# Optimization experiments

Hardware: AMD Instinct MI355X
Metric: run time of the kernel (lower is better)

Reference implementation:

```python
import jax, jax.numpy as jnp
import numpy as np

D_MODEL = 512
OUT = 512
D_STATE = 16
D_CONV = 4
EXPAND = 2
N_LAYERS = 2
D_INNER = EXPAND * D_MODEL
DT_RANK = -(-D_MODEL // 16)  # ceil(d_model/16) = 32
B = 2
L = 2048


def setup_inputs() -> dict:
    key = jax.random.key(0)
    ks = jax.random.split(key, 16)
    def w(k, shape, scale):
        return jax.random.normal(k, shape, dtype=jnp.float32) * scale
    s_d = 1.0 / np.sqrt(D_MODEL)
    s_e = 1.0 / np.sqrt(D_INNER)
    s_r = 1.0 / np.sqrt(DT_RANK)
    s_f = 1.0 / np.sqrt(2 * D_MODEL)
    return {
        "x": jax.random.normal(ks[0], (B, L, D_MODEL), dtype=jnp.float32),
        "in_proj_w": w(ks[1], (N_LAYERS, 2 * D_INNER, D_MODEL), s_d),
        "conv_w": w(ks[2], (N_LAYERS, D_INNER, D_CONV), 0.5),
        "conv_b": jnp.zeros((N_LAYERS, D_INNER), jnp.float32),
        "x_proj_w": w(ks[3], (N_LAYERS, DT_RANK + 2 * D_STATE, D_INNER), s_e),
        "dt_w": w(ks[4], (N_LAYERS, D_INNER, DT_RANK), s_r),
        "dt_b": w(ks[5], (N_LAYERS, D_INNER), 0.1),
        "A_log": jnp.tile(jnp.log(jnp.arange(1, D_STATE + 1, dtype=jnp.float32))[None, None, :], (N_LAYERS, D_INNER, 1)),
        "Dp": jnp.ones((N_LAYERS, D_INNER), jnp.float32),
        "out_proj_w": w(ks[6], (N_LAYERS, D_MODEL, D_INNER), s_e),
        "rms_w": jnp.ones((N_LAYERS, D_MODEL), jnp.float32),
        "ln1_w": jnp.ones((D_MODEL,), jnp.float32),
        "ln1_b": jnp.zeros((D_MODEL,), jnp.float32),
        "ln2_w": jnp.ones((D_MODEL,), jnp.float32),
        "ln2_b": jnp.zeros((D_MODEL,), jnp.float32),
        "ffn_w1": w(ks[7], (2 * D_MODEL, D_MODEL), s_d),
        "ffn_b1": jnp.zeros((2 * D_MODEL,), jnp.float32),
        "ffn_w2": w(ks[8], (D_MODEL, 2 * D_MODEL), s_f),
        "ffn_b2": jnp.zeros((D_MODEL,), jnp.float32),
        "final_w": w(ks[9], (OUT, D_MODEL), s_d),
        "final_b": jnp.zeros((OUT,), jnp.float32),
    }


def _ln(x, w, b, eps=1e-5):
    mu = x.mean(-1, keepdims=True)
    v = ((x - mu) ** 2).mean(-1, keepdims=True)
    return (x - mu) * jax.lax.rsqrt(v + eps) * w + b


def _rms(x, w, eps=1e-5):
    return x * jax.lax.rsqrt(jnp.mean(x * x, -1, keepdims=True) + eps) * w


def _mixer(x, ipw, cw, cb, xpw, dtw, dtb, alog, dpar, opw):
    # x: [B, L, D]; single Mamba mixer (in_proj -> causal depthwise conv -> SSM -> gate -> out_proj)
    Lx = x.shape[1]
    xz = x @ ipw.T                              # [B, L, 2*ED]
    xc, z = jnp.split(xz, 2, axis=-1)
    xp = jnp.pad(xc, ((0, 0), (D_CONV - 1, 0), (0, 0)))  # causal left-pad
    xc = cb + sum(cw[:, k] * xp[:, k:k + Lx, :] for k in range(D_CONV))
    xc = jax.nn.silu(xc)
    dbc = xc @ xpw.T                            # [B, L, dt_rank + 2*N]
    delta = jax.nn.softplus(dbc[..., :DT_RANK] @ dtw.T + dtb)   # [B, L, ED]
    Bm = dbc[..., DT_RANK:DT_RANK + D_STATE]    # [B, L, N]
    Cm = dbc[..., DT_RANK + D_STATE:]           # [B, L, N]
    A = -jnp.exp(alog)                          # [ED, N]
    dA = jnp.exp(delta[..., None] * A)          # [B, L, ED, N]
    dBx = (delta * xc)[..., None] * Bm[:, :, None, :]  # [B, L, ED, N]
    def step(h, inp):
        a, bx = inp
        h = a * h + bx
        return h, h
    _, hs = jax.lax.scan(step, jnp.zeros_like(dA[:, 0]), (jnp.moveaxis(dA, 1, 0), jnp.moveaxis(dBx, 1, 0)))
    hs = jnp.moveaxis(hs, 0, 1)                 # [B, L, ED, N]
    y = jnp.einsum('blen,bln->ble', hs, Cm) + dpar * xc
    return (y * jax.nn.silu(z)) @ opw.T


def _forward(x, in_proj_w, conv_w, conv_b, x_proj_w, dt_w, dt_b, A_log, Dp, out_proj_w, rms_w,
             ln1_w, ln1_b, ln2_w, ln2_b, ffn_w1, ffn_b1, ffn_w2, ffn_b2, final_w, final_b):
    h = _ln(x, ln1_w, ln1_b)
    for i in range(N_LAYERS):  # Mamba = stack of residual RMSNorm+mixer blocks
        h = h + _mixer(_rms(h, rms_w[i]), in_proj_w[i], conv_w[i], conv_b[i], x_proj_w[i],
                       dt_w[i], dt_b[i], A_log[i], Dp[i], out_proj_w[i])
    x = x + h
    f = jax.nn.relu(_ln(x, ln2_w, ln2_b) @ ffn_w1.T + ffn_b1) @ ffn_w2.T + ffn_b2
    x = x + f
    return x @ final_w.T + final_b


def reference(x, in_proj_w, conv_w, conv_b, x_proj_w, dt_w, dt_b, A_log, Dp, out_proj_w, rms_w,
              ln1_w, ln1_b, ln2_w, ln2_b, ffn_w1, ffn_b1, ffn_w2, ffn_b2, final_w, final_b):
    return _forward(x, in_proj_w, conv_w, conv_b, x_proj_w, dt_w, dt_b, A_log, Dp, out_proj_w, rms_w,
                    ln1_w, ln1_b, ln2_w, ln2_b, ffn_w1, ffn_b1, ffn_w2, ffn_b2, final_w, final_b)
```

## Files before the change

### kernel.cpp

```cpp
#include <hip/hip_runtime.h>
#include <math.h>

#define ROWS 4096
#define LSEQ 2048
#define DM   512
#define DI   1024
#define NCH  64
#define CHT  (LSEQ / NCH)
#define NCOMB 1152

typedef __bf16 bf16_t;
typedef bf16_t bf16x8 __attribute__((ext_vector_type(8)));
typedef float f32x4 __attribute__((ext_vector_type(4)));
typedef unsigned int u32;
typedef const __attribute__((address_space(1))) u32* gp32;
typedef __attribute__((address_space(3))) u32* lp32;

__device__ __forceinline__ float siluf(float v) { return v / (1.f + expf(-v)); }
__device__ __forceinline__ float softplusf(float v) {
    return fmaxf(v, 0.f) + log1pf(expf(-fabsf(v)));
}

template <bool OUTBF>
__global__ __launch_bounds__(256) void ln_kernel(const float* __restrict__ x,
                                                 const float* __restrict__ w,
                                                 const float* __restrict__ b,
                                                 void* __restrict__ outv) {
    int row = blockIdx.x;
    int tid = threadIdx.x;
    const float* xr = x + (size_t)row * DM;
    float v0 = xr[tid], v1 = xr[tid + 256];
    float sum = v0 + v1, sq = v0 * v0 + v1 * v1;
    for (int o = 32; o > 0; o >>= 1) {
        sum += __shfl_down(sum, o);
        sq  += __shfl_down(sq, o);
    }
    __shared__ float s1[4], s2[4];
    int wid = tid >> 6, lane = tid & 63;
    if (lane == 0) { s1[wid] = sum; s2[wid] = sq; }
    __syncthreads();
    sum = s1[0] + s1[1] + s1[2] + s1[3];
    sq  = s2[0] + s2[1] + s2[2] + s2[3];
    float mu  = sum * (1.f / DM);
    float var = sq * (1.f / DM) - mu * mu;
    float r   = rsqrtf(var + 1e-5f);
    float o0 = (v0 - mu) * r * w[tid] + b[tid];
    float o1 = (v1 - mu) * r * w[tid + 256] + b[tid + 256];
    if (OUTBF) {
        bf16_t* out = (bf16_t*)outv;
        out[(size_t)row * DM + tid]       = (bf16_t)o0;
        out[(size_t)row * DM + tid + 256] = (bf16_t)o1;
    } else {
        float* out = (float*)outv;
        out[(size_t)row * DM + tid]       = o0;
        out[(size_t)row * DM + tid + 256] = o1;
    }
}

__global__ __launch_bounds__(256) void rms_kernel(const float* __restrict__ x,
                                                  const float* __restrict__ w,
                                                  bf16_t* __restrict__ out) {
    int row = blockIdx.x;
    int tid = threadIdx.x;
    const float* xr = x + (size_t)row * DM;
    float v0 = xr[tid], v1 = xr[tid + 256];
    float sq = v0 * v0 + v1 * v1;
    for (int o = 32; o > 0; o >>= 1) sq += __shfl_down(sq, o);
    __shared__ float s2[4];
    int wid = tid >> 6, lane = tid & 63;
    if (lane == 0) s2[wid] = sq;
    __syncthreads();
    sq = s2[0] + s2[1] + s2[2] + s2[3];
    float r = rsqrtf(sq * (1.f / DM) + 1e-5f);
    out[(size_t)row * DM + tid]       = (bf16_t)(v0 * r * w[tid]);
    out[(size_t)row * DM + tid + 256] = (bf16_t)(v1 * r * w[tid + 256]);
}

__global__ __launch_bounds__(256) void cvt_kernel(
    const float* __restrict__ ipw, const float* __restrict__ opw,
    const float* __restrict__ fw1, const float* __restrict__ fw2,
    const float* __restrict__ finw, bf16_t* __restrict__ arena) {
    int idx = blockIdx.x * 256 + threadIdx.x;
    float v;
    if (idx < 2097152)      v = ipw[idx];
    else if (idx < 3145728) v = opw[idx - 2097152];
    else if (idx < 3670016) v = fw1[idx - 3145728];
    else if (idx < 4194304) v = fw2[idx - 3670016];
    else                    v = finw[idx - 4194304];
    arena[idx] = (bf16_t)v;
}

__global__ __launch_bounds__(256) void wd_kernel(
    const float* __restrict__ dtw, const float* __restrict__ xpw,
    bf16_t* __restrict__ wcomb) {
    int idx = blockIdx.x * 256 + threadIdx.x;
    int j = idx & 1023;
    int i = idx >> 10;
    float v;
    if (i < 1024) {
        const float* dr = dtw + i * 32;
        v = 0.f;
#pragma unroll
        for (int k = 0; k < 32; ++k) v = fmaf(dr[k], xpw[k * 1024 + j], v);
    } else if (i < 1056) {
        v = xpw[(i - 1024 + 32) * 1024 + j];
    } else {
        v = 0.f;
    }
    wcomb[idx] = (bf16_t)v;
}

template <int ACT, bool BIAS, bool RES, bool OUTBF>
__global__ __launch_bounds__(256) void mgemm_kernel(
    const bf16_t* __restrict__ A, const bf16_t* __restrict__ W,
    const float* __restrict__ bias, const float* __restrict__ res,
    void* __restrict__ Cv, int M, int N, int K, int ldc,
    const bf16_t* __restrict__ xcp, float* __restrict__ dxc,
    float* __restrict__ bcb, void* __restrict__ aux) {
    __shared__ bf16_t As[128 * 64];
    __shared__ bf16_t Bs[128 * 64];
    const int tid  = threadIdx.x;
    const int lane = tid & 63;
    const int wave = tid >> 6;
    const int wr = wave >> 1, wc = wave & 1;
    const int bm = blockIdx.y * 128, bn = blockIdx.x * 128;
    const int l16 = lane & 15, kgrp = lane >> 4;
    const int prow = tid >> 3;
    const int pp   = tid & 7;
    const int wbase = (tid & ~63) * 8;

    f32x4 acc[4][4] = {};

    for (int k0 = 0; k0 < K; k0 += 64) {
        __syncthreads();
#pragma unroll
        for (int it = 0; it < 4; ++it) {
            int r  = it * 32 + prow;
            int gc = k0 + ((pp ^ (r & 7)) << 3);
            const bf16_t* ga = A + (size_t)(bm + r) * K + gc;
            const bf16_t* gb = W + (size_t)(bn + r) * K + gc;
            __builtin_amdgcn_global_load_lds((gp32)(const void*)ga,
                (lp32)(void*)(As + it * 2048 + wbase), 16, 0, 0);
            __builtin_amdgcn_global_load_lds((gp32)(const void*)gb,
                (lp32)(void*)(Bs + it * 2048 + wbase), 16, 0, 0);
        }
        __syncthreads();
#pragma unroll
        for (int ks = 0; ks < 2; ++ks) {
            bf16x8 af[4], bv[4];
#pragma unroll
            for (int i = 0; i < 4; ++i) {
                int ra = wr * 64 + i * 16 + l16;
                int rb = wc * 64 + i * 16 + l16;
                af[i] = *(const bf16x8*)(As + ra * 64 + ((((ks << 2) | kgrp) ^ (ra & 7)) << 3));
                bv[i] = *(const bf16x8*)(Bs + rb * 64 + ((((ks << 2) | kgrp) ^ (rb & 7)) << 3));
            }
#pragma unroll
            for (int i = 0; i < 4; ++i)
#pragma unroll
                for (int j = 0; j < 4; ++j)
                    acc[i][j] = __builtin_amdgcn_mfma_f32_16x16x32_bf16(
                        af[i], bv[j], acc[i][j], 0, 0, 0);
        }
    }
#pragma unroll
    for (int i = 0; i < 4; ++i) {
#pragma unroll
        for (int j = 0; j < 4; ++j) {
            int col = bn + wc * 64 + j * 16 + l16;
            if (ACT == 2) {
                if (col < 1024) {
                    float badd = bias[col];
#pragma unroll
                    for (int q = 0; q < 4; ++q) {
                        int row = bm + wr * 64 + i * 16 + kgrp * 4 + q;
                        float d = softplusf(acc[i][j][q] + badd);
                        ((float*)Cv)[(size_t)row * 1024 + col] = d;
                        dxc[(size_t)row * 1024 + col] =
                            d * (float)xcp[(size_t)row * 1024 + col];
                    }
                } else if (col < 1056) {
#pragma unroll
                    for (int q = 0; q < 4; ++q) {
                        int row = bm + wr * 64 + i * 16 + kgrp * 4 + q;
                        bcb[(size_t)row * 32 + (col - 1024)] = acc[i][j][q];
                    }
                }
            } else if (ACT == 3) {
#pragma unroll
                for (int q = 0; q < 4; ++q) {
                    int row = bm + wr * 64 + i * 16 + kgrp * 4 + q;
                    float v = acc[i][j][q];
                    if (col < 1024)
                        ((float*)Cv)[(size_t)row * 1024 + col] = v;
                    else
                        ((bf16_t*)aux)[(size_t)row * 1024 + (col - 1024)] = (bf16_t)v;
                }
            } else {
                float badd = BIAS ? bias[col] : 0.f;
#pragma unroll
                for (int q = 0; q < 4; ++q) {
                    int row = bm + wr * 64 + i * 16 + kgrp * 4 + q;
                    float v = acc[i][j][q] + badd;
                    if (RES) v += res[(size_t)row * ldc + col];
                    if (ACT == 1) v = fmaxf(v, 0.f);
                    if (OUTBF) ((bf16_t*)Cv)[(size_t)row * ldc + col] = (bf16_t)v;
                    else       ((float*)Cv)[(size_t)row * ldc + col] = v;
                }
            }
        }
    }
}

__global__ __launch_bounds__(256) void conv_silu_kernel(
    const float* __restrict__ xraw, const float* __restrict__ cw,
    const float* __restrict__ cb, bf16_t* __restrict__ out) {
    int idx = blockIdx.x * blockDim.x + threadIdx.x;
    int c = idx & (DI - 1);
    int row = idx >> 10;
    int t = row & (LSEQ - 1);
    float acc = cb[c];
#pragma unroll
    for (int k = 0; k < 4; ++k) {
        int st = t + k - 3;
        if (st >= 0) acc = fmaf(cw[c * 4 + k], xraw[(size_t)(row + k - 3) * 1024 + c], acc);
    }
    out[idx] = (bf16_t)siluf(acc);
}

__global__ __launch_bounds__(256) void scan1_kernel(
    const float* __restrict__ dbuf, const float* __restrict__ dxcb,
    const float* __restrict__ bc_in, const float* __restrict__ A_log,
    float* __restrict__ aprod, float* __restrict__ bacc) {
    int gid  = blockIdx.x * 256 + threadIdx.x;
    int e    = gid >> 1;
    int half = gid & 1;
    int ch = blockIdx.y;
    int b  = blockIdx.z;
    float cAn[8];
#pragma unroll
    for (int n = 0; n < 8; ++n)
        cAn[n] = -expf(A_log[e * 16 + half * 8 + n]) * 1.4426950408889634f;
    float ap[8], bc[8];
#pragma unroll
    for (int n = 0; n < 8; ++n) { ap[n] = 1.f; bc[n] = 0.f; }
    int row0 = b * LSEQ + ch * CHT;
    float d_c   = dbuf[(size_t)row0 * DI + e];
    float dxc_c = dxcb[(size_t)row0 * 1024 + e];
    for (int t = 0; t < CHT; ++t) {
        int row = row0 + t;
        float d_n = 0.f, dxc_n = 0.f;
        if (t + 1 < CHT) {
            d_n   = dbuf[(size_t)(row + 1) * DI + e];
            dxc_n = dxcb[(size_t)(row + 1) * 1024 + e];
        }
        const float* brow = bc_in + (size_t)row * 32 + half * 8;
        float4 b0 = *(const float4*)brow;
        float4 b1 = *(const float4*)(brow + 4);
        float Bn[8] = {b0.x, b0.y, b0.z, b0.w, b1.x, b1.y, b1.z, b1.w};
#pragma unroll
        for (int n = 0; n < 8; ++n) {
            float dA = exp2f(d_c * cAn[n]);
            ap[n] *= dA;
            bc[n] = fmaf(dA, bc[n], dxc_c * Bn[n]);
        }
        d_c = d_n; dxc_c = dxc_n;
    }
    size_t idx = ((size_t)((b * NCH + ch) * DI + e)) * 16 + half * 8;
    float4* apo = (float4*)(aprod + idx);
    float4* bco = (float4*)(bacc + idx);
#pragma unroll
    for (int q = 0; q < 2; ++q) {
        apo[q] = make_float4(ap[q * 4], ap[q * 4 + 1], ap[q * 4 + 2], ap[q * 4 + 3]);
        bco[q] = make_float4(bc[q * 4], bc[q * 4 + 1], bc[q * 4 + 2], bc[q * 4 + 3]);
    }
}

__global__ __launch_bounds__(256) void scan2_kernel(
    const float* aprod, const float* bacc, float* hinit) {
    int tid = blockIdx.x * 256 + threadIdx.x;
    int n = tid & 15;
    int e = (tid >> 4) & (DI - 1);
    int b = tid >> 14;
    float h = 0.f;
    for (int ch = 0; ch < NCH; ++ch) {
        size_t idx = ((size_t)((b * NCH + ch) * DI + e)) * 16 + n;
        float a  = aprod[idx];
        float bb = bacc[idx];
        hinit[idx] = h;
        h = fmaf(a, h, bb);
    }
}

__global__ __launch_bounds__(256) void scan3_kernel(
    const float* __restrict__ dbuf, const float* __restrict__ dxcb,
    const bf16_t* __restrict__ xcb, const bf16_t* __restrict__ zb,
    const float* __restrict__ bc_in, const float* __restrict__ A_log,
    const float* __restrict__ Dp, const float* __restrict__ hinit,
    bf16_t* __restrict__ yg) {
    int gid  = blockIdx.x * 256 + threadIdx.x;
    int e    = gid >> 1;
    int half = gid & 1;
    int ch = blockIdx.y;
    int b  = blockIdx.z;
    float cAn[8];
#pragma unroll
    for (int n = 0; n < 8; ++n)
        cAn[n] = -expf(A_log[e * 16 + half * 8 + n]) * 1.4426950408889634f;
    float h[8];
    {
        const float4* hp = (const float4*)(hinit +
            ((size_t)((b * NCH + ch) * DI + e)) * 16 + half * 8);
#pragma unroll
        for (int q = 0; q < 2; ++q) {
            float4 v = hp[q];
            h[q * 4] = v.x; h[q * 4 + 1] = v.y; h[q * 4 + 2] = v.z; h[q * 4 + 3] = v.w;
        }
    }
    float Dpe = Dp[e];
    int row0 = b * LSEQ + ch * CHT;
    float d_c   = dbuf[(size_t)row0 * DI + e];
    float dxc_c = dxcb[(size_t)row0 * 1024 + e];
    float xc_c  = (float)xcb[(size_t)row0 * 1024 + e];
    float z_c   = (float)zb[(size_t)row0 * 1024 + e];
    for (int t = 0; t < CHT; ++t) {
        int row = row0 + t;
        float d_n = 0.f, dxc_n = 0.f, xc_n = 0.f, z_n = 0.f;
        if (t + 1 < CHT) {
            d_n   = dbuf[(size_t)(row + 1) * DI + e];
            dxc_n = dxcb[(size_t)(row + 1) * 1024 + e];
            xc_n  = (float)xcb[(size_t)(row + 1) * 1024 + e];
            z_n   = (float)zb[(size_t)(row + 1) * 1024 + e];
        }
        const float* brow = bc_in + (size_t)row * 32;
        float4 b0 = *(const float4*)(brow + half * 8);
        float4 b1 = *(const float4*)(brow + half * 8 + 4);
        float4 c0 = *(const float4*)(brow + 16 + half * 8);
        float4 c1 = *(const float4*)(brow + 16 + half * 8 + 4);
        float Bn[8] = {b0.x, b0.y, b0.z, b0.w, b1.x, b1.y, b1.z, b1.w};
        float Cn[8] = {c0.x, c0.y, c0.z, c0.w, c1.x, c1.y, c1.z, c1.w};
        float y = half ? 0.f : Dpe * xc_c;
#pragma unroll
        for (int n = 0; n < 8; ++n) {
            float dA = exp2f(d_c * cAn[n]);
            h[n] = fmaf(dA, h[n], dxc_c * Bn[n]);
            y = fmaf(h[n], Cn[n], y);
        }
        y += __shfl_xor(y, 1);
        if (half == 0)
            yg[(size_t)row * DI + e] = (bf16_t)(y * siluf(z_c));
        d_c = d_n; dxc_c = dxc_n; xc_c = xc_n; z_c = z_n;
    }
}

__global__ __launch_bounds__(256) void add_kernel(const float* __restrict__ a,
                                                  const float* __restrict__ b,
                                                  float* __restrict__ c, int n) {
    int i = blockIdx.x * blockDim.x + threadIdx.x;
    if (i < n) c[i] = a[i] + b[i];
}

extern "C" void kernel_launch(void* const* d_in, const int* in_sizes, int n_in,
                              void* d_out, int out_size, void* d_ws, size_t ws_size,
                              hipStream_t stream) {
    const float* x    = (const float*)d_in[0];
    const float* ipw  = (const float*)d_in[1];
    const float* cw   = (const float*)d_in[2];
    const float* cb   = (const float*)d_in[3];
    const float* xpw  = (const float*)d_in[4];
    const float* dtw  = (const float*)d_in[5];
    const float* dtb  = (const float*)d_in[6];
    const float* alog = (const float*)d_in[7];
    const float* dpar = (const float*)d_in[8];
    const float* opw  = (const float*)d_in[9];
    const float* rmsw = (const float*)d_in[10];
    const float* ln1w = (const float*)d_in[11];
    const float* ln1b = (const float*)d_in[12];
    const float* ln2w = (const float*)d_in[13];
    const float* ln2b = (const float*)d_in[14];
    const float* fw1  = (const float*)d_in[15];
    const float* fb1  = (const float*)d_in[16];
    const float* fw2  = (const float*)d_in[17];
    const float* fb2  = (const float*)d_in[18];
    const float* finw = (const float*)d_in[19];
    const float* finb = (const float*)d_in[20];
    float* out = (float*)d_out;

    const size_t MF = 1u << 20;
    float*  ws    = (float*)d_ws;
    float*  h     = ws;
    bf16_t* hnb   = (bf16_t*)(ws + 2 * MF);
    float*  xdx   = ws + 3 * MF;
    bf16_t* zb    = (bf16_t*)(ws + 7 * MF);
    bf16_t* xcb   = (bf16_t*)(ws + 9 * MF);
    float*  bcbuf = ws + 11 * MF;
    float*  dbuf  = ws + 11 * MF + MF / 8;
    float*  shab  = ws + 15 * MF + MF / 8;
    float*  aprod = ws + 17 * MF + MF / 8;
    bf16_t* warena = (bf16_t*)(ws + 19 * MF + MF / 8);
    float*  bacc  = shab;
    bf16_t* ygb   = (bf16_t*)shab;
    float*  hinit = aprod;
    const size_t IPW_OFF = 0, OPW_OFF = 2097152, FW1_OFF = 3145728,
                 FW2_OFF = 3670016, FINW_OFF = 4194304, WC_OFF = 4456448;

    cvt_kernel<<<17408, 256, 0, stream>>>(ipw, opw, fw1, fw2, finw, warena);
    for (int i = 0; i < 2; ++i)
        wd_kernel<<<NCOMB * 1024 / 256, 256, 0, stream>>>(
            dtw + (size_t)i * DI * 32, xpw + (size_t)i * 64 * DI,
            warena + WC_OFF + (size_t)i * NCOMB * 1024);
    ln_kernel<false><<<ROWS, 256, 0, stream>>>(x, ln1w, ln1b, h);

    for (int i = 0; i < 2; ++i) {
        const bf16_t* ipwb_i = warena + IPW_OFF + (size_t)i * 2048 * 512;
        const bf16_t* opwb_i = warena + OPW_OFF + (size_t)i * 512 * 1024;
        const bf16_t* wcombb = warena + WC_OFF + (size_t)i * NCOMB * 1024;
        const float* cw_i   = cw   + (size_t)i * DI * 4;
        const float* cb_i   = cb   + (size_t)i * DI;
        const float* dtb_i  = dtb  + (size_t)i * DI;
        const float* alog_i = alog + (size_t)i * DI * 16;
        const float* dp_i   = dpar + (size_t)i * DI;
        const float* rms_i  = rmsw + (size_t)i * DM;

        rms_kernel<<<ROWS, 256, 0, stream>>>(h, rms_i, hnb);
        mgemm_kernel<3, false, false, false><<<dim3(16, 32), 256, 0, stream>>>(
            hnb, ipwb_i, nullptr, nullptr, xdx, ROWS, 2048, 512, 1024,
            nullptr, nullptr, nullptr, zb);
        conv_silu_kernel<<<ROWS * DI / 256, 256, 0, stream>>>(xdx, cw_i, cb_i, xcb);
        mgemm_kernel<2, false, false, false><<<dim3(NCOMB / 128, 32), 256, 0, stream>>>(
            xcb, wcombb, dtb_i, nullptr, dbuf, ROWS, NCOMB, 1024, 1024,
            xcb, xdx, bcbuf, nullptr);
        scan1_kernel<<<dim3(8, NCH, 2), 256, 0, stream>>>(dbuf, xdx, bcbuf, alog_i,
                                                          aprod, bacc);
        scan2_kernel<<<128, 256, 0, stream>>>(aprod, bacc, hinit);
        scan3_kernel<<<dim3(8, NCH, 2), 256, 0, stream>>>(dbuf, xdx, xcb, zb, bcbuf,
                                                          alog_i, dp_i, hinit, ygb);
        mgemm_kernel<0, false, true, false><<<dim3(4, 32), 256, 0, stream>>>(
            ygb, opwb_i, nullptr, h, h, ROWS, DM, 1024, DM,
            nullptr, nullptr, nullptr, nullptr);
    }

    float* x2 = dbuf;
    add_kernel<<<ROWS * DM / 256, 256, 0, stream>>>(x, h, x2, ROWS * DM);
    ln_kernel<true><<<ROWS, 256, 0, stream>>>(x2, ln2w, ln2b, hnb);
    bf16_t* midb = (bf16_t*)xdx;
    mgemm_kernel<1, true, false, true><<<dim3(8, 32), 256, 0, stream>>>(
        hnb, warena + FW1_OFF, fb1, nullptr, midb, ROWS, DI, 512, DI,
        nullptr, nullptr, nullptr, nullptr);
    bf16_t* x3b = zb;
    mgemm_kernel<0, true, true, true><<<dim3(4, 32), 256, 0, stream>>>(
        midb, warena + FW2_OFF, fb2, x2, x3b, ROWS, DM, 1024, DM,
        nullptr, nullptr, nullptr, nullptr);
    mgemm_kernel<0, true, false, false><<<dim3(4, 32), 256, 0, stream>>>(
        x3b, warena + FINW_OFF, finb, nullptr, out, ROWS, DM, 512, DM,
        nullptr, nullptr, nullptr, nullptr);
}
```

Baseline: 568.7 us.

## Store intermediates in bf16, shrink GEMM tiles, parallelize scan2, fuse add+LN

Several changes at once. Intermediates that were fp32 (x_raw, delta, delta*xc) are now stored in bf16. The GEMM gets a templated M tile of 64 rows with a 1D grid and an XCD-aware block remap, which raises block counts. The serial inter-chunk scan is split into three more parallel hierarchical kernels. The residual add is fused into the second LayerNorm. Together these cut memory traffic and improve occupancy, at the cost of bf16 rounding on delta and the conv input.

```diff
diff --git a/kernel.cpp b/kernel.cpp
--- a/kernel.cpp
+++ b/kernel.cpp
@@ -21,11 +21,10 @@
     return fmaxf(v, 0.f) + log1pf(expf(-fabsf(v)));
 }
 
-template <bool OUTBF>
 __global__ __launch_bounds__(256) void ln_kernel(const float* __restrict__ x,
                                                  const float* __restrict__ w,
                                                  const float* __restrict__ b,
-                                                 void* __restrict__ outv) {
+                                                 float* __restrict__ out) {
     int row = blockIdx.x;
     int tid = threadIdx.x;
     const float* xr = x + (size_t)row * DM;
@@ -44,17 +43,37 @@
     float mu  = sum * (1.f / DM);
     float var = sq * (1.f / DM) - mu * mu;
     float r   = rsqrtf(var + 1e-5f);
-    float o0 = (v0 - mu) * r * w[tid] + b[tid];
-    float o1 = (v1 - mu) * r * w[tid + 256] + b[tid + 256];
-    if (OUTBF) {
-        bf16_t* out = (bf16_t*)outv;
-        out[(size_t)row * DM + tid]       = (bf16_t)o0;
-        out[(size_t)row * DM + tid + 256] = (bf16_t)o1;
-    } else {
-        float* out = (float*)outv;
-        out[(size_t)row * DM + tid]       = o0;
-        out[(size_t)row * DM + tid + 256] = o1;
-    }
+    out[(size_t)row * DM + tid]       = (v0 - mu) * r * w[tid] + b[tid];
+    out[(size_t)row * DM + tid + 256] = (v1 - mu) * r * w[tid + 256] + b[tid + 256];
+}
+
+__global__ __launch_bounds__(256) void ln_add_kernel(
+    const float* __restrict__ x, const float* __restrict__ hres,
+    const float* __restrict__ w, const float* __restrict__ b,
+    float* __restrict__ x2, bf16_t* __restrict__ outb) {
+    int row = blockIdx.x;
+    int tid = threadIdx.x;
+    size_t base = (size_t)row * DM;
+    float v0 = x[base + tid] + hres[base + tid];
+    float v1 = x[base + tid + 256] + hres[base + tid + 256];
+    x2[base + tid] = v0;
+    x2[base + tid + 256] = v1;
+    float sum = v0 + v1, sq = v0 * v0 + v1 * v1;
+    for (int o = 32; o > 0; o >>= 1) {
+        sum += __shfl_down(sum, o);
+        sq  += __shfl_down(sq, o);
+    }
+    __shared__ float s1[4], s2[4];
+    int wid = tid >> 6, lane = tid & 63;
+    if (lane == 0) { s1[wid] = sum; s2[wid] = sq; }
+    __syncthreads();
+    sum = s1[0] + s1[1] + s1[2] + s1[3];
+    sq  = s2[0] + s2[1] + s2[2] + s2[3];
+    float mu  = sum * (1.f / DM);
+    float var = sq * (1.f / DM) - mu * mu;
+    float r   = rsqrtf(var + 1e-5f);
+    outb[base + tid]       = (bf16_t)((v0 - mu) * r * w[tid] + b[tid]);
+    outb[base + tid + 256] = (bf16_t)((v1 - mu) * r * w[tid + 256] + b[tid + 256]);
 }
 
 __global__ __launch_bounds__(256) void rms_kernel(const float* __restrict__ x,
@@ -110,53 +129,65 @@
     wcomb[idx] = (bf16_t)v;
 }
 
-template <int ACT, bool BIAS, bool RES, bool OUTBF>
+template <int BMF, int ACT, bool BIAS, bool RES, bool OUTBF>
 __global__ __launch_bounds__(256) void mgemm_kernel(
     const bf16_t* __restrict__ A, const bf16_t* __restrict__ W,
     const float* __restrict__ bias, const float* __restrict__ res,
-    void* __restrict__ Cv, int M, int N, int K, int ldc,
-    const bf16_t* __restrict__ xcp, float* __restrict__ dxc,
+    void* __restrict__ Cv, int nbn, int K, int ldc,
+    const bf16_t* __restrict__ xcp, bf16_t* __restrict__ dxc,
     float* __restrict__ bcb, void* __restrict__ aux) {
-    __shared__ bf16_t As[128 * 64];
+    constexpr int BM = BMF * 32;
+    __shared__ bf16_t As[BM * 64];
     __shared__ bf16_t Bs[128 * 64];
     const int tid  = threadIdx.x;
     const int lane = tid & 63;
     const int wave = tid >> 6;
     const int wr = wave >> 1, wc = wave & 1;
-    const int bm = blockIdx.y * 128, bn = blockIdx.x * 128;
     const int l16 = lane & 15, kgrp = lane >> 4;
     const int prow = tid >> 3;
     const int pp   = tid & 7;
     const int wbase = (tid & ~63) * 8;
-
-    f32x4 acc[4][4] = {};
+    const int cpx = (int)gridDim.x >> 3;
+    const int id  = ((int)blockIdx.x & 7) * cpx + ((int)blockIdx.x >> 3);
+    const int bn  = (id % nbn) * 128;
+    const int bm  = (id / nbn) * BM;
+
+    f32x4 acc[BMF][4] = {};
 
     for (int k0 = 0; k0 < K; k0 += 64) {
         __syncthreads();
+#pragma unroll
+        for (int it = 0; it < BMF; ++it) {
+            int r  = it * 32 + prow;
+            int gc = k0 + ((pp ^ (r & 7)) << 3);
+            __builtin_amdgcn_global_load_lds(
+                (gp32)(const void*)(A + (size_t)(bm + r) * K + gc),
+                (lp32)(void*)(As + it * 2048 + wbase), 16, 0, 0);
+        }
 #pragma unroll
         for (int it = 0; it < 4; ++it) {
             int r  = it * 32 + prow;
             int gc = k0 + ((pp ^ (r & 7)) << 3);
-            const bf16_t* ga = A + (size_t)(bm + r) * K + gc;
-            const bf16_t* gb = W + (size_t)(bn + r) * K + gc;
-            __builtin_amdgcn_global_load_lds((gp32)(const void*)ga,
-                (lp32)(void*)(As + it * 2048 + wbase), 16, 0, 0);
-            __builtin_amdgcn_global_load_lds((gp32)(const void*)gb,
+            __builtin_amdgcn_global_load_lds(
+                (gp32)(const void*)(W + (size_t)(bn + r) * K + gc),
                 (lp32)(void*)(Bs + it * 2048 + wbase), 16, 0, 0);
         }
         __syncthreads();
 #pragma unroll
         for (int ks = 0; ks < 2; ++ks) {
-            bf16x8 af[4], bv[4];
-#pragma unroll
-            for (int i = 0; i < 4; ++i) {
-                int ra = wr * 64 + i * 16 + l16;
-                int rb = wc * 64 + i * 16 + l16;
+            bf16x8 af[BMF], bv[4];
+#pragma unroll
+            for (int i = 0; i < BMF; ++i) {
+                int ra = wr * (BM / 2) + i * 16 + l16;
                 af[i] = *(const bf16x8*)(As + ra * 64 + ((((ks << 2) | kgrp) ^ (ra & 7)) << 3));
-                bv[i] = *(const bf16x8*)(Bs + rb * 64 + ((((ks << 2) | kgrp) ^ (rb & 7)) << 3));
             }
 #pragma unroll
-            for (int i = 0; i < 4; ++i)
+            for (int j = 0; j < 4; ++j) {
+                int rb = wc * 64 + j * 16 + l16;
+                bv[j] = *(const bf16x8*)(Bs + rb * 64 + ((((ks << 2) | kgrp) ^ (rb & 7)) << 3));
+            }
+#pragma unroll
+            for (int i = 0; i < BMF; ++i)
 #pragma unroll
                 for (int j = 0; j < 4; ++j)
                     acc[i][j] = __builtin_amdgcn_mfma_f32_16x16x32_bf16(
@@ -164,7 +195,7 @@
         }
     }
 #pragma unroll
-    for (int i = 0; i < 4; ++i) {
+    for (int i = 0; i < BMF; ++i) {
 #pragma unroll
         for (int j = 0; j < 4; ++j) {
             int col = bn + wc * 64 + j * 16 + l16;
@@ -173,26 +204,26 @@
                     float badd = bias[col];
 #pragma unroll
                     for (int q = 0; q < 4; ++q) {
-                        int row = bm + wr * 64 + i * 16 + kgrp * 4 + q;
+                        int row = bm + wr * (BM / 2) + i * 16 + kgrp * 4 + q;
                         float d = softplusf(acc[i][j][q] + badd);
-                        ((float*)Cv)[(size_t)row * 1024 + col] = d;
+                        ((bf16_t*)Cv)[(size_t)row * 1024 + col] = (bf16_t)d;
                         dxc[(size_t)row * 1024 + col] =
-                            d * (float)xcp[(size_t)row * 1024 + col];
+                            (bf16_t)(d * (float)xcp[(size_t)row * 1024 + col]);
                     }
                 } else if (col < 1056) {
 #pragma unroll
                     for (int q = 0; q < 4; ++q) {
-                        int row = bm + wr * 64 + i * 16 + kgrp * 4 + q;
+                        int row = bm + wr * (BM / 2) + i * 16 + kgrp * 4 + q;
                         bcb[(size_t)row * 32 + (col - 1024)] = acc[i][j][q];
                     }
                 }
             } else if (ACT == 3) {
 #pragma unroll
                 for (int q = 0; q < 4; ++q) {
-                    int row = bm + wr * 64 + i * 16 + kgrp * 4 + q;
+                    int row = bm + wr * (BM / 2) + i * 16 + kgrp * 4 + q;
                     float v = acc[i][j][q];
                     if (col < 1024)
-                        ((float*)Cv)[(size_t)row * 1024 + col] = v;
+                        ((bf16_t*)Cv)[(size_t)row * 1024 + col] = (bf16_t)v;
                     else
                         ((bf16_t*)aux)[(size_t)row * 1024 + (col - 1024)] = (bf16_t)v;
                 }
@@ -200,7 +231,7 @@
                 float badd = BIAS ? bias[col] : 0.f;
 #pragma unroll
                 for (int q = 0; q < 4; ++q) {
-                    int row = bm + wr * 64 + i * 16 + kgrp * 4 + q;
+                    int row = bm + wr * (BM / 2) + i * 16 + kgrp * 4 + q;
                     float v = acc[i][j][q] + badd;
                     if (RES) v += res[(size_t)row * ldc + col];
                     if (ACT == 1) v = fmaxf(v, 0.f);
@@ -213,7 +244,7 @@
 }
 
 __global__ __launch_bounds__(256) void conv_silu_kernel(
-    const float* __restrict__ xraw, const float* __restrict__ cw,
+    const bf16_t* __restrict__ xraw, const float* __restrict__ cw,
     const float* __restrict__ cb, bf16_t* __restrict__ out) {
     int idx = blockIdx.x * blockDim.x + threadIdx.x;
     int c = idx & (DI - 1);
@@ -223,13 +254,14 @@
 #pragma unroll
     for (int k = 0; k < 4; ++k) {
         int st = t + k - 3;
-        if (st >= 0) acc = fmaf(cw[c * 4 + k], xraw[(size_t)(row + k - 3) * 1024 + c], acc);
+        if (st >= 0)
+            acc = fmaf(cw[c * 4 + k], (float)xraw[(size_t)(row + k - 3) * 1024 + c], acc);
     }
     out[idx] = (bf16_t)siluf(acc);
 }
 
 __global__ __launch_bounds__(256) void scan1_kernel(
-    const float* __restrict__ dbuf, const float* __restrict__ dxcb,
+    const bf16_t* __restrict__ dbuf, const bf16_t* __restrict__ dxcb,
     const float* __restrict__ bc_in, const float* __restrict__ A_log,
     float* __restrict__ aprod, float* __restrict__ bacc) {
     int gid  = blockIdx.x * 256 + threadIdx.x;
@@ -245,14 +277,14 @@
 #pragma unroll
     for (int n = 0; n < 8; ++n) { ap[n] = 1.f; bc[n] = 0.f; }
     int row0 = b * LSEQ + ch * CHT;
-    float d_c   = dbuf[(size_t)row0 * DI + e];
-    float dxc_c = dxcb[(size_t)row0 * 1024 + e];
+    float d_c   = (float)dbuf[(size_t)row0 * DI + e];
+    float dxc_c = (float)dxcb[(size_t)row0 * 1024 + e];
     for (int t = 0; t < CHT; ++t) {
         int row = row0 + t;
         float d_n = 0.f, dxc_n = 0.f;
         if (t + 1 < CHT) {
-            d_n   = dbuf[(size_t)(row + 1) * DI + e];
-            dxc_n = dxcb[(size_t)(row + 1) * 1024 + e];
+            d_n   = (float)dbuf[(size_t)(row + 1) * DI + e];
+            dxc_n = (float)dxcb[(size_t)(row + 1) * 1024 + e];
         }
         const float* brow = bc_in + (size_t)row * 32 + half * 8;
         float4 b0 = *(const float4*)brow;
@@ -276,24 +308,51 @@
     }
 }
 
-__global__ __launch_bounds__(256) void scan2_kernel(
-    const float* aprod, const float* bacc, float* hinit) {
-    int tid = blockIdx.x * 256 + threadIdx.x;
-    int n = tid & 15;
-    int e = (tid >> 4) & (DI - 1);
-    int b = tid >> 14;
+__global__ __launch_bounds__(256) void scan2a_kernel(
+    const float* __restrict__ aprod, const float* __restrict__ bacc,
+    float* __restrict__ gA, float* __restrict__ gB) {
+    int t = blockIdx.x * 256 + threadIdx.x;
+    int n = t & 15, e = (t >> 4) & 1023, grp = (t >> 14) & 7, b = t >> 17;
+    float A = 1.f, B = 0.f;
+    for (int i = 0; i < 8; ++i) {
+        int ch = grp * 8 + i;
+        size_t idx = ((size_t)((b * NCH + ch) * DI + e)) * 16 + n;
+        float a = aprod[idx], bb = bacc[idx];
+        A = a * A;
+        B = fmaf(a, B, bb);
+    }
+    size_t g = ((size_t)((b * 8 + grp) * DI + e)) * 16 + n;
+    gA[g] = A; gB[g] = B;
+}
+__global__ __launch_bounds__(256) void scan2b_kernel(
+    const float* __restrict__ gA, const float* __restrict__ gB,
+    float* __restrict__ ghin) {
+    int t = blockIdx.x * 256 + threadIdx.x;
+    int n = t & 15, e = (t >> 4) & 1023, b = t >> 14;
     float h = 0.f;
-    for (int ch = 0; ch < NCH; ++ch) {
+    for (int g = 0; g < 8; ++g) {
+        size_t idx = ((size_t)((b * 8 + g) * DI + e)) * 16 + n;
+        ghin[idx] = h;
+        h = fmaf(gA[idx], h, gB[idx]);
+    }
+}
+__global__ __launch_bounds__(256) void scan2c_kernel(
+    const float* __restrict__ ghin, float* aprod_hinit,
+    const float* __restrict__ bacc) {
+    int t = blockIdx.x * 256 + threadIdx.x;
+    int n = t & 15, e = (t >> 4) & 1023, grp = (t >> 14) & 7, b = t >> 17;
+    float h = ghin[((size_t)((b * 8 + grp) * DI + e)) * 16 + n];
+    for (int i = 0; i < 8; ++i) {
+        int ch = grp * 8 + i;
         size_t idx = ((size_t)((b * NCH + ch) * DI + e)) * 16 + n;
-        float a  = aprod[idx];
-        float bb = bacc[idx];
-        hinit[idx] = h;
+        float a = aprod_hinit[idx], bb = bacc[idx];
+        aprod_hinit[idx] = h;
         h = fmaf(a, h, bb);
     }
 }
 
 __global__ __launch_bounds__(256) void scan3_kernel(
-    const float* __restrict__ dbuf, const float* __restrict__ dxcb,
+    const bf16_t* __restrict__ dbuf, const bf16_t* __restrict__ dxcb,
     const bf16_t* __restrict__ xcb, const bf16_t* __restrict__ zb,
     const float* __restrict__ bc_in, const float* __restrict__ A_log,
     const float* __restrict__ Dp, const float* __restrict__ hinit,
@@ -319,16 +378,16 @@
     }
     float Dpe = Dp[e];
     int row0 = b * LSEQ + ch * CHT;
-    float d_c   = dbuf[(size_t)row0 * DI + e];
-    float dxc_c = dxcb[(size_t)row0 * 1024 + e];
+    float d_c   = (float)dbuf[(size_t)row0 * DI + e];
+    float dxc_c = (float)dxcb[(size_t)row0 * 1024 + e];
     float xc_c  = (float)xcb[(size_t)row0 * 1024 + e];
     float z_c   = (float)zb[(size_t)row0 * 1024 + e];
     for (int t = 0; t < CHT; ++t) {
         int row = row0 + t;
         float d_n = 0.f, dxc_n = 0.f, xc_n = 0.f, z_n = 0.f;
         if (t + 1 < CHT) {
-            d_n   = dbuf[(size_t)(row + 1) * DI + e];
-            dxc_n = dxcb[(size_t)(row + 1) * 1024 + e];
+            d_n   = (float)dbuf[(size_t)(row + 1) * DI + e];
+            dxc_n = (float)dxcb[(size_t)(row + 1) * 1024 + e];
             xc_n  = (float)xcb[(size_t)(row + 1) * 1024 + e];
             z_n   = (float)zb[(size_t)(row + 1) * 1024 + e];
         }
@@ -351,13 +410,6 @@
             yg[(size_t)row * DI + e] = (bf16_t)(y * siluf(z_c));
         d_c = d_n; dxc_c = dxc_n; xc_c = xc_n; z_c = z_n;
     }
-}
-
-__global__ __launch_bounds__(256) void add_kernel(const float* __restrict__ a,
-                                                  const float* __restrict__ b,
-                                                  float* __restrict__ c, int n) {
-    int i = blockIdx.x * blockDim.x + threadIdx.x;
-    if (i < n) c[i] = a[i] + b[i];
 }
 
 extern "C" void kernel_launch(void* const* d_in, const int* in_sizes, int n_in,
@@ -387,20 +439,26 @@
     float* out = (float*)d_out;
 
     const size_t MF = 1u << 20;
-    float*  ws    = (float*)d_ws;
-    float*  h     = ws;
-    bf16_t* hnb   = (bf16_t*)(ws + 2 * MF);
-    float*  xdx   = ws + 3 * MF;
-    bf16_t* zb    = (bf16_t*)(ws + 7 * MF);
-    bf16_t* xcb   = (bf16_t*)(ws + 9 * MF);
-    float*  bcbuf = ws + 11 * MF;
-    float*  dbuf  = ws + 11 * MF + MF / 8;
-    float*  shab  = ws + 15 * MF + MF / 8;
-    float*  aprod = ws + 17 * MF + MF / 8;
-    bf16_t* warena = (bf16_t*)(ws + 19 * MF + MF / 8);
-    float*  bacc  = shab;
-    bf16_t* ygb   = (bf16_t*)shab;
-    float*  hinit = aprod;
+    float*  ws     = (float*)d_ws;
+    float*  h      = ws;
+    bf16_t* hnb    = (bf16_t*)(ws + 2 * MF);
+    bf16_t* xrawb  = (bf16_t*)(ws + 3 * MF);
+    bf16_t* zb     = (bf16_t*)(ws + 5 * MF);
+    bf16_t* xcb    = (bf16_t*)(ws + 7 * MF);
+    bf16_t* dbufb  = (bf16_t*)(ws + 9 * MF);
+    bf16_t* dxcbb  = (bf16_t*)(ws + 11 * MF);
+    float*  bcbuf  = ws + 13 * MF;
+    bf16_t* ygb    = (bf16_t*)(ws + 13 * MF + MF / 4);
+    float*  aprod  = ws + 15 * MF + MF / 4;
+    float*  bacc   = ws + 17 * MF + MF / 4;
+    float*  gsA    = ws + 19 * MF + MF / 4;
+    float*  gsB    = ws + 19 * MF + MF / 2;
+    float*  ghin   = ws + 19 * MF + 3 * MF / 4;
+    bf16_t* warena = (bf16_t*)(ws + 20 * MF);
+    float*  x2     = (float*)dbufb;
+    bf16_t* midb   = xcb;
+    bf16_t* x3b    = dxcbb;
+    float*  hinit  = aprod;
     const size_t IPW_OFF = 0, OPW_OFF = 2097152, FW1_OFF = 3145728,
                  FW2_OFF = 3670016, FINW_OFF = 4194304, WC_OFF = 4456448;
 
@@ -409,7 +467,7 @@
         wd_kernel<<<NCOMB * 1024 / 256, 256, 0, stream>>>(
             dtw + (size_t)i * DI * 32, xpw + (size_t)i * 64 * DI,
             warena + WC_OFF + (size_t)i * NCOMB * 1024);
-    ln_kernel<false><<<ROWS, 256, 0, stream>>>(x, ln1w, ln1b, h);
+    ln_kernel<<<ROWS, 256, 0, stream>>>(x, ln1w, ln1b, h);
 
     for (int i = 0; i < 2; ++i) {
         const bf16_t* ipwb_i = warena + IPW_OFF + (size_t)i * 2048 * 512;
@@ -423,35 +481,34 @@
         const float* rms_i  = rmsw + (size_t)i * DM;
 
         rms_kernel<<<ROWS, 256, 0, stream>>>(h, rms_i, hnb);
-        mgemm_kernel<3, false, false, false><<<dim3(16, 32), 256, 0, stream>>>(
-            hnb, ipwb_i, nullptr, nullptr, xdx, ROWS, 2048, 512, 1024,
+        mgemm_kernel<2, 3, false, false, false><<<1024, 256, 0, stream>>>(
+            hnb, ipwb_i, nullptr, nullptr, xrawb, 16, 512, 1024,
             nullptr, nullptr, nullptr, zb);
-        conv_silu_kernel<<<ROWS * DI / 256, 256, 0, stream>>>(xdx, cw_i, cb_i, xcb);
-        mgemm_kernel<2, false, false, false><<<dim3(NCOMB / 128, 32), 256, 0, stream>>>(
-            xcb, wcombb, dtb_i, nullptr, dbuf, ROWS, NCOMB, 1024, 1024,
-            xcb, xdx, bcbuf, nullptr);
-        scan1_kernel<<<dim3(8, NCH, 2), 256, 0, stream>>>(dbuf, xdx, bcbuf, alog_i,
-                                                          aprod, bacc);
-        scan2_kernel<<<128, 256, 0, stream>>>(aprod, bacc, hinit);
-        scan3_kernel<<<dim3(8, NCH, 2), 256, 0, stream>>>(dbuf, xdx, xcb, zb, bcbuf,
-                                                          alog_i, dp_i, hinit, ygb);
-        mgemm_kernel<0, false, true, false><<<dim3(4, 32), 256, 0, stream>>>(
-            ygb, opwb_i, nullptr, h, h, ROWS, DM, 1024, DM,
+        conv_silu_kernel<<<ROWS * DI / 256, 256, 0, stream>>>(xrawb, cw_i, cb_i, xcb);
+        mgemm_kernel<2, 2, false, false, false><<<576, 256, 0, stream>>>(
+            xcb, wcombb, dtb_i, nullptr, dbufb, 9, 1024, 1024,
+            xcb, dxcbb, bcbuf, nullptr);
+        scan1_kernel<<<dim3(8, NCH, 2), 256, 0, stream>>>(dbufb, dxcbb, bcbuf,
+                                                          alog_i, aprod, bacc);
+        scan2a_kernel<<<1024, 256, 0, stream>>>(aprod, bacc, gsA, gsB);
+        scan2b_kernel<<<128, 256, 0, stream>>>(gsA, gsB, ghin);
+        scan2c_kernel<<<1024, 256, 0, stream>>>(ghin, aprod, bacc);
+        scan3_kernel<<<dim3(8, NCH, 2), 256, 0, stream>>>(dbufb, dxcbb, xcb, zb,
+                                                          bcbuf, alog_i, dp_i,
+                                                          hinit, ygb);
+        mgemm_kernel<2, 0, false, true, false><<<256, 256, 0, stream>>>(
+            ygb, opwb_i, nullptr, h, h, 4, 1024, DM,
             nullptr, nullptr, nullptr, nullptr);
     }
 
-    float* x2 = dbuf;
-    add_kernel<<<ROWS * DM / 256, 256, 0, stream>>>(x, h, x2, ROWS * DM);
-    ln_kernel<true><<<ROWS, 256, 0, stream>>>(x2, ln2w, ln2b, hnb);
-    bf16_t* midb = (bf16_t*)xdx;
-    mgemm_kernel<1, true, false, true><<<dim3(8, 32), 256, 0, stream>>>(
-        hnb, warena + FW1_OFF, fb1, nullptr, midb, ROWS, DI, 512, DI,
+    ln_add_kernel<<<ROWS, 256, 0, stream>>>(x, h, ln2w, ln2b, x2, hnb);
+    mgemm_kernel<2, 1, true, false, true><<<512, 256, 0, stream>>>(
+        hnb, warena + FW1_OFF, fb1, nullptr, midb, 8, 512, DI,
         nullptr, nullptr, nullptr, nullptr);
-    bf16_t* x3b = zb;
-    mgemm_kernel<0, true, true, true><<<dim3(4, 32), 256, 0, stream>>>(
-        midb, warena + FW2_OFF, fb2, x2, x3b, ROWS, DM, 1024, DM,
+    mgemm_kernel<2, 0, true, true, true><<<256, 256, 0, stream>>>(
+        midb, warena + FW2_OFF, fb2, x2, x3b, 4, 1024, DM,
         nullptr, nullptr, nullptr, nullptr);
-    mgemm_kernel<0, true, false, false><<<dim3(4, 32), 256, 0, stream>>>(
-        x3b, warena + FINW_OFF, finb, nullptr, out, ROWS, DM, 512, DM,
+    mgemm_kernel<2, 0, true, false, false><<<256, 256, 0, stream>>>(
+        x3b, warena + FINW_OFF, finb, nullptr, out, 4, 512, DM,
         nullptr, nullptr, nullptr, nullptr);
 }
```

Result: faster. 512.1 us (-10.0%).
